# Performance work log

Measured on AMD Instinct MI355X. Metric: run time of the kernel, lower is better.

Reference implementation:

```python
import jax, jax.numpy as jnp
import numpy as np

N = 100000          # nodes
E = 3200000         # edges (avg degree 32)
EPS = 1e-5          # BatchNorm eps
SLOPE = 0.01        # LeakyReLU negative slope


def _glorot(key, shape):
    lim = float(np.sqrt(6.0 / (shape[0] + shape[1])))
    return jax.random.uniform(key, shape, jnp.float32, -lim, lim)


def setup_inputs() -> dict:
    key = jax.random.key(0)
    ks = jax.random.split(key, 8)
    x = jax.random.normal(ks[0], (N, 128), jnp.float32)
    edge_index = jax.random.randint(ks[1], (2, E), 0, N, dtype=jnp.int64)
    W1 = _glorot(ks[2], (128, 256)); b1 = jnp.zeros((256,), jnp.float32)
    W2 = _glorot(ks[3], (256, 512)); b2 = jnp.zeros((512,), jnp.float32)
    g1 = jnp.ones((256,), jnp.float32); be1 = jnp.zeros((256,), jnp.float32)
    g2 = jnp.ones((512,), jnp.float32); be2 = jnp.zeros((512,), jnp.float32)
    Wd1 = _glorot(ks[4], (512, 4096)); bd1 = jnp.zeros((4096,), jnp.float32)
    Wd2 = _glorot(ks[5], (4096, 6)); bd2 = jnp.zeros((6,), jnp.float32)
    return dict(x=x, edge_index=edge_index, W1=W1, b1=b1, W2=W2, b2=b2,
                g1=g1, be1=be1, g2=g2, be2=be2,
                Wd1=Wd1, bd1=bd1, Wd2=Wd2, bd2=bd2)


def gcn_conv(x, src, dst, W, b):
    # PyG GCNConv: x' = D^{-1/2} (A + I) D^{-1/2} (x W) + b
    n = x.shape[0]
    xw = x @ W                                   # [N, out]
    loop = jnp.arange(n, dtype=src.dtype)
    s = jnp.concatenate([src, loop])             # add self-loops
    d = jnp.concatenate([dst, loop])
    deg = jax.ops.segment_sum(jnp.ones_like(d, dtype=x.dtype), d, num_segments=n)
    dinv = jnp.where(deg > 0, jax.lax.rsqrt(deg), 0.0)
    norm = dinv[s] * dinv[d]                     # [E+N]
    out = jax.ops.segment_sum(xw[s] * norm[:, None], d, num_segments=n)
    return out + b


def batchnorm(x, g, b):
    # training-mode BN over node dim, biased variance (as torch)
    m = x.mean(axis=0)
    v = x.var(axis=0)
    return (x - m) * jax.lax.rsqrt(v + EPS) * g + b


def leaky_relu(x):
    return jnp.where(x >= 0, x, SLOPE * x)


def reference(x, edge_index, W1, b1, W2, b2, g1, be1, g2, be2, Wd1, bd1, Wd2, bd2):
    src, dst = edge_index[0], edge_index[1]
    y = leaky_relu(batchnorm(gcn_conv(x, src, dst, W1, b1), g1, be1))
    y = leaky_relu(batchnorm(gcn_conv(y, src, dst, W2, b2), g2, be2))
    y = leaky_relu(y @ Wd1 + bd1)
    y = y @ Wd2 + bd2
    return jax.nn.softmax(y, axis=1)
```

## Files before the change

### kernel.cpp

```cpp
#include <hip/hip_runtime.h>
#include <math.h>

#define LEAKY(t) ((t) >= 0.0f ? (t) : 0.01f * (t))

typedef __attribute__((ext_vector_type(8))) short bf16x8;
typedef __attribute__((ext_vector_type(4))) float f32x4;

static __device__ __forceinline__ float b2f(unsigned short u) {
    return __uint_as_float(((unsigned)u) << 16);
}
static __device__ __forceinline__ unsigned short f2b(float f) {
    unsigned x = __float_as_uint(f);
    unsigned r = (x + 0x7fffu + ((x >> 16) & 1u)) >> 16;
    return (unsigned short)r;
}


__global__ void k_seti(int* __restrict__ p, int v, int n) {
    int i = blockIdx.x * blockDim.x + threadIdx.x;
    int st = gridDim.x * blockDim.x;
    for (; i < n; i += st) p[i] = v;
}

__global__ void k_setf(float* __restrict__ p, float v, int n) {
    int i = blockIdx.x * blockDim.x + threadIdx.x;
    int st = gridDim.x * blockDim.x;
    for (; i < n; i += st) p[i] = v;
}

__global__ void k_stash_b16(const unsigned short* __restrict__ a, int i0, int i1, int i2, int i3,
                            float* __restrict__ dst) {
    if (threadIdx.x == 0 && blockIdx.x == 0) {
        dst[0] = b2f(a[i0]); dst[1] = b2f(a[i1]); dst[2] = b2f(a[i2]); dst[3] = b2f(a[i3]);
    }
}


__global__ void k_cvt(const float* __restrict__ src, unsigned short* __restrict__ dst,
                      long long n4) {
    long long i = (long long)blockIdx.x * blockDim.x + threadIdx.x;
    long long st = (long long)gridDim.x * blockDim.x;
    for (; i < n4; i += st) {
        float4 v = *(const float4*)(src + 4 * i);
        ushort4 o;
        o.x = f2b(v.x); o.y = f2b(v.y); o.z = f2b(v.z); o.w = f2b(v.w);
        *(ushort4*)(dst + 4 * i) = o;
    }
}


__global__ void k_detect(const int* __restrict__ ei, int* __restrict__ flag) {
    __shared__ int nz;
    if (threadIdx.x == 0) nz = 0;
    __syncthreads();
    int acc = 0;
    for (int i = threadIdx.x; i < 1024; i += 256) acc |= ei[2 * i + 1];
    if (acc != 0) atomicOr(&nz, 1);
    __syncthreads();
    if (threadIdx.x == 0) *flag = (nz == 0) ? 1 : 0;
}


__global__ void k_count(const int* __restrict__ ei, int E, int Nn,
                        const int* __restrict__ flag, int* __restrict__ cnt) {
    int f = *flag;
    int i = blockIdx.x * blockDim.x + threadIdx.x;
    int stride = gridDim.x * blockDim.x;
    for (; i < E; i += stride) {
        int d = f ? ei[2 * E + 2 * i] : ei[E + i];
        if ((unsigned)d < (unsigned)Nn) atomicAdd(&cnt[d], 1);
    }
}

__global__ void k_dinv(const int* __restrict__ cnt, float* __restrict__ dinv, int n) {
    int i = blockIdx.x * blockDim.x + threadIdx.x;
    if (i < n) dinv[i] = rsqrtf((float)(cnt[i] + 1));
}

__global__ void k_scan(const int* __restrict__ cnt, int* __restrict__ start, int n) {
    __shared__ int sm[256];
    __shared__ int carry;
    int tid = threadIdx.x;
    if (tid == 0) carry = 0;
    __syncthreads();
    for (int base = 0; base < n; base += 1024) {
        int i0 = base + tid * 4;
        int v0 = (i0 + 0 < n) ? cnt[i0 + 0] : 0;
        int v1 = (i0 + 1 < n) ? cnt[i0 + 1] : 0;
        int v2 = (i0 + 2 < n) ? cnt[i0 + 2] : 0;
        int v3 = (i0 + 3 < n) ? cnt[i0 + 3] : 0;
        int s = v0 + v1 + v2 + v3;
        sm[tid] = s;
        __syncthreads();
        int x = s;
        for (int off = 1; off < 256; off <<= 1) {
            int y = (tid >= off) ? sm[tid - off] : 0;
            __syncthreads();
            x += y;
            sm[tid] = x;
            __syncthreads();
        }
        int e = x - s + carry;
        if (i0 + 0 < n) start[i0 + 0] = e; e += v0;
        if (i0 + 1 < n) start[i0 + 1] = e; e += v1;
        if (i0 + 2 < n) start[i0 + 2] = e; e += v2;
        if (i0 + 3 < n) start[i0 + 3] = e; e += v3;
        __syncthreads();
        if (tid == 255) carry += sm[255];
        __syncthreads();
    }
    if (tid == 0) start[n] = carry;
}

__global__ void k_copy_i32(const int* __restrict__ a, int* __restrict__ b, int n) {
    int i = blockIdx.x * blockDim.x + threadIdx.x;
    if (i < n) b[i] = a[i];
}

__global__ void k_fill(const int* __restrict__ ei, int E, int Nn,
                       const int* __restrict__ flag,
                       int* __restrict__ cursor, int* __restrict__ srcS) {
    int f = *flag;
    int i = blockIdx.x * blockDim.x + threadIdx.x;
    int stride = gridDim.x * blockDim.x;
    for (; i < E; i += stride) {
        int s = f ? ei[2 * i] : ei[i];
        int d = f ? ei[2 * E + 2 * i] : ei[E + i];
        if ((unsigned)d < (unsigned)Nn) {
            int p = atomicAdd(&cursor[d], 1);
            srcS[p] = ((unsigned)s < (unsigned)Nn) ? s : 0;
        }
    }
}


__global__ void k_aggb(const unsigned short* __restrict__ X, const float* __restrict__ dinv,
                       const int* __restrict__ start, const int* __restrict__ srcS,
                       unsigned short* __restrict__ out, int F, int M) {
    int t = threadIdx.x;
    for (int n = blockIdx.x; n < M; n += gridDim.x) {
        float di = dinv[n];
        unsigned v = *(const unsigned*)(X + (size_t)n * F + 2 * t);
        float a0 = b2f((unsigned short)(v & 0xffff)) * di;
        float a1 = b2f((unsigned short)(v >> 16)) * di;
        int j = start[n], e1 = start[n + 1];
        for (; j + 1 < e1; j += 2) {
            int s0 = srcS[j], s1 = srcS[j + 1];
            float w0 = dinv[s0], w1 = dinv[s1];
            unsigned u0 = *(const unsigned*)(X + (size_t)s0 * F + 2 * t);
            unsigned u1 = *(const unsigned*)(X + (size_t)s1 * F + 2 * t);
            a0 += b2f((unsigned short)(u0 & 0xffff)) * w0;
            a1 += b2f((unsigned short)(u0 >> 16)) * w0;
            a0 += b2f((unsigned short)(u1 & 0xffff)) * w1;
            a1 += b2f((unsigned short)(u1 >> 16)) * w1;
        }
        if (j < e1) {
            int s0 = srcS[j];
            float w0 = dinv[s0];
            unsigned u0 = *(const unsigned*)(X + (size_t)s0 * F + 2 * t);
            a0 += b2f((unsigned short)(u0 & 0xffff)) * w0;
            a1 += b2f((unsigned short)(u0 >> 16)) * w0;
        }
        unsigned o = (unsigned)f2b(a0 * di) | ((unsigned)f2b(a1 * di) << 16);
        *(unsigned*)(out + (size_t)n * F + 2 * t) = o;
    }
}


__global__ __launch_bounds__(256, 2)
void k_gemm1(const unsigned short* __restrict__ A, const unsigned short* __restrict__ W1s,
             unsigned short* __restrict__ C, int M) {
    int tid = threadIdx.x;
    int lane = tid & 63, w = tid >> 6;
    int lr = lane & 15, lg = lane >> 4;
    int row0 = blockIdx.x * 64;
    int arow = row0 + w * 16 + lr;
    const unsigned short* Ar = A + (size_t)(arow < M ? arow : (M - 1)) * 128;
    bf16x8 a8[4];
#pragma unroll
    for (int ko = 0; ko < 4; ko++)
        a8[ko] = *(const bf16x8*)(Ar + ko * 32 + lg * 8);
    for (int ct = 0; ct < 16; ct += 2) {
        f32x4 acc0 = {0.f, 0.f, 0.f, 0.f}, acc1 = {0.f, 0.f, 0.f, 0.f};
#pragma unroll
        for (int ko = 0; ko < 4; ko++) {
            const unsigned short* bp = W1s + ((size_t)(ct * 4 + ko) * 64 + lane) * 8;
            bf16x8 b0 = *(const bf16x8*)bp;
            bf16x8 b1 = *(const bf16x8*)(bp + 2048);
            acc0 = __builtin_amdgcn_mfma_f32_16x16x32_bf16(a8[ko], b0, acc0, 0, 0, 0);
            acc1 = __builtin_amdgcn_mfma_f32_16x16x32_bf16(a8[ko], b1, acc1, 0, 0, 0);
        }
        int col = ct * 16 + lr;
#pragma unroll
        for (int i = 0; i < 4; i++) {
            int r = row0 + w * 16 + lg * 4 + i;
            if (r < M) {
                C[(size_t)r * 256 + col] = f2b(acc0[i]);
                C[(size_t)r * 256 + col + 16] = f2b(acc1[i]);
            }
        }
    }
}


__global__ void k_gemm2stats(const unsigned short* __restrict__ T2,
                             const unsigned short* __restrict__ W2s,
                             float* __restrict__ sums, int M) {
    __shared__ float ls[512];
    __shared__ float lq[512];
    int tid = threadIdx.x;
    int lane = tid & 63, w = tid >> 6;
    int lr = lane & 15, lg = lane >> 4;
    int row0 = blockIdx.x * 64;
    for (int i = tid; i < 512; i += 256) { ls[i] = 0.f; lq[i] = 0.f; }
    __syncthreads();

    int arow = row0 + w * 16 + lr;
    bf16x8 a8[8];
    if (arow < M) {
        const unsigned short* T2r = T2 + (size_t)arow * 256;
#pragma unroll
        for (int ko = 0; ko < 8; ko++)
            a8[ko] = *(const bf16x8*)(T2r + ko * 32 + lg * 8);
    } else {
#pragma unroll
        for (int ko = 0; ko < 8; ko++)
            a8[ko] = (bf16x8){0, 0, 0, 0, 0, 0, 0, 0};
    }

    for (int ct = 0; ct < 32; ct += 2) {
        f32x4 acc0 = {0.f, 0.f, 0.f, 0.f}, acc1 = {0.f, 0.f, 0.f, 0.f};
#pragma unroll
        for (int ko = 0; ko < 8; ko++) {
            const unsigned short* bp = W2s + ((size_t)(ct * 8 + ko) * 64 + lane) * 8;
            bf16x8 b0 = *(const bf16x8*)bp;
            bf16x8 b1 = *(const bf16x8*)(bp + 4096);
            acc0 = __builtin_amdgcn_mfma_f32_16x16x32_bf16(a8[ko], b0, acc0, 0, 0, 0);
            acc1 = __builtin_amdgcn_mfma_f32_16x16x32_bf16(a8[ko], b1, acc1, 0, 0, 0);
        }
        float s0 = 0.f, q0 = 0.f, s1 = 0.f, q1 = 0.f;
#pragma unroll
        for (int i = 0; i < 4; i++) {
            float y0 = acc0[i]; s0 += y0; q0 += y0 * y0;
            float y1 = acc1[i]; s1 += y1; q1 += y1 * y1;
        }
        s0 += __shfl_xor(s0, 16); s0 += __shfl_xor(s0, 32);
        q0 += __shfl_xor(q0, 16); q0 += __shfl_xor(q0, 32);
        s1 += __shfl_xor(s1, 16); s1 += __shfl_xor(s1, 32);
        q1 += __shfl_xor(q1, 16); q1 += __shfl_xor(q1, 32);
        if (lg == 0) {
            atomicAdd(&ls[ct * 16 + lr], s0);
            atomicAdd(&lq[ct * 16 + lr], q0);
            atomicAdd(&ls[(ct + 1) * 16 + lr], s1);
            atomicAdd(&lq[(ct + 1) * 16 + lr], q1);
        }
    }
    __syncthreads();
    for (int c = tid; c < 512; c += 256) {
        atomicAdd(&sums[c], ls[c]);
        atomicAdd(&sums[512 + c], lq[c]);
    }
}


__global__ void k_bnparam(float* __restrict__ sums, const float* __restrict__ g,
                          const float* __restrict__ be, int n, int F) {
    int c = blockIdx.x * blockDim.x + threadIdx.x;
    if (c < F) {
        float m = sums[c] / n;
        float v = sums[F + c] / n - m * m;
        float a = g[c] * rsqrtf(v + 1e-5f);
        sums[c] = a;
        sums[F + c] = be[c] - m * a;
    }
}

__global__ void k_colstats_b16(const unsigned short* __restrict__ X, float* __restrict__ sums, int n) {
    int t = threadIdx.x;
    int r0 = blockIdx.x * 256;
    int r1 = min(r0 + 256, n);
    float s = 0.f, q = 0.f;
    for (int r = r0; r < r1; r++) {
        float v = b2f(X[(size_t)r * 256 + t]);
        s += v; q += v * v;
    }
    atomicAdd(&sums[t], s);
    atomicAdd(&sums[256 + t], q);
}

__global__ void k_bnleaky_b16(unsigned short* __restrict__ X, const float* __restrict__ p,
                              long long total) {
    long long i = (long long)blockIdx.x * blockDim.x + threadIdx.x;
    long long stride = (long long)gridDim.x * blockDim.x;
    for (; i < total; i += stride) {
        int c = (int)(i & 255);
        float y = b2f(X[i]) * p[c] + p[256 + c];
        X[i] = f2b(LEAKY(y));
    }
}


__global__ void k_swz(const float* __restrict__ src, unsigned short* __restrict__ dst,
                      int N, int KO) {
    __shared__ float t[32][65];
    int tid = threadIdx.x;
    int ko = blockIdx.x;
    int n0 = blockIdx.y * 64;
    int r = tid >> 3, c8 = (tid & 7) * 8;
    const float* s = src + (size_t)(ko * 32 + r) * N + n0 + c8;
    float4 v0 = *(const float4*)s;
    float4 v1 = *(const float4*)(s + 4);
    t[r][c8 + 0] = v0.x; t[r][c8 + 1] = v0.y; t[r][c8 + 2] = v0.z; t[r][c8 + 3] = v0.w;
    t[r][c8 + 4] = v1.x; t[r][c8 + 5] = v1.y; t[r][c8 + 6] = v1.z; t[r][c8 + 7] = v1.w;
    __syncthreads();
    int cc = tid >> 6, lane = tid & 63;
    int lr = lane & 15, lg = lane >> 4;
    int ct = (n0 >> 4) + cc;
    bf16x8 ov;
#pragma unroll
    for (int j = 0; j < 8; j++) ov[j] = (short)f2b(t[lg * 8 + j][cc * 16 + lr]);
    *(bf16x8*)(dst + ((size_t)(ct * KO + ko) * 64 + lane) * 8) = ov;
}


__global__ __launch_bounds__(512, 1)
void k_dense(const unsigned short* __restrict__ T2,
             const unsigned short* __restrict__ W2s,
             const float* __restrict__ bnp,
             const float* __restrict__ bd1,
             const unsigned short* __restrict__ Wd1s,
             const float* __restrict__ Wd2,
             float* __restrict__ logits, int M) {
    __shared__ unsigned short Y2f[8 * 8192];
    __shared__ float sl[2][128][6];
    int tid = threadIdx.x;
    int lane = tid & 63, w = tid >> 6;
    int lr = lane & 15, lg = lane >> 4;
    int row0 = blockIdx.x * 128;

    int arow = row0 + w * 16 + lr;
    const unsigned short* T2r = T2 + (size_t)(arow < M ? arow : (M - 1)) * 256;
    bf16x8 a8[8];
#pragma unroll
    for (int ko = 0; ko < 8; ko++)
        a8[ko] = *(const bf16x8*)(T2r + ko * 32 + lg * 8);
    for (int ct = 0; ct < 32; ct += 2) {
        f32x4 acc0 = {0.f, 0.f, 0.f, 0.f}, acc1 = {0.f, 0.f, 0.f, 0.f};
#pragma unroll
        for (int ko = 0; ko < 8; ko++) {
            const unsigned short* bp = W2s + ((size_t)(ct * 8 + ko) * 64 + lane) * 8;
            bf16x8 b0 = *(const bf16x8*)bp;
            bf16x8 b1 = *(const bf16x8*)(bp + 4096);
            acc0 = __builtin_amdgcn_mfma_f32_16x16x32_bf16(a8[ko], b0, acc0, 0, 0, 0);
            acc1 = __builtin_amdgcn_mfma_f32_16x16x32_bf16(a8[ko], b1, acc1, 0, 0, 0);
        }
        int col = ct * 16 + lr;
        float sc0 = bnp[col], sh0 = bnp[512 + col];
        float sc1 = bnp[col + 16], sh1 = bnp[512 + col + 16];
        int koa = ct >> 1;
        int lgb = lr >> 3;
        int jj = lr & 7;
        int base = w * 8192 + (koa * 64 + lgb * 16) * 8 + jj;
#pragma unroll
        for (int i = 0; i < 4; i++) {
            int r16 = lg * 4 + i;
            float y0 = fmaf(acc0[i], sc0, sh0); y0 = LEAKY(y0);
            Y2f[base + r16 * 8] = f2b(y0);
            float y1 = fmaf(acc1[i], sc1, sh1); y1 = LEAKY(y1);
            Y2f[base + (32 * 8) + r16 * 8] = f2b(y1);
        }
    }
    __syncthreads();

    int rg = w & 3, ch = w >> 2;
    const unsigned short* fA = Y2f + (size_t)(2 * rg) * 8192;
    const unsigned short* fB = Y2f + (size_t)(2 * rg + 1) * 8192;
    float l0[4][6] = {{0.f}}, l1[4][6] = {{0.f}};
    int ct0 = ch * 128;
    for (int ct = ct0; ct < ct0 + 128; ct += 2) {
        f32x4 aA0 = {0.f, 0.f, 0.f, 0.f}, aA1 = {0.f, 0.f, 0.f, 0.f};
        f32x4 aB0 = {0.f, 0.f, 0.f, 0.f}, aB1 = {0.f, 0.f, 0.f, 0.f};
#pragma unroll
        for (int ko = 0; ko < 16; ko++) {
            const unsigned short* bp = Wd1s + ((size_t)(ct * 16 + ko) * 64 + lane) * 8;
            bf16x8 b0 = *(const bf16x8*)bp;
            bf16x8 b1 = *(const bf16x8*)(bp + 8192);
            bf16x8 pa = *(const bf16x8*)(fA + (ko * 64 + lane) * 8);
            bf16x8 pb = *(const bf16x8*)(fB + (ko * 64 + lane) * 8);
            aA0 = __builtin_amdgcn_mfma_f32_16x16x32_bf16(pa, b0, aA0, 0, 0, 0);
            aA1 = __builtin_amdgcn_mfma_f32_16x16x32_bf16(pa, b1, aA1, 0, 0, 0);
            aB0 = __builtin_amdgcn_mfma_f32_16x16x32_bf16(pb, b0, aB0, 0, 0, 0);
            aB1 = __builtin_amdgcn_mfma_f32_16x16x32_bf16(pb, b1, aB1, 0, 0, 0);
        }
#define EPI(C, AA, BB) { \
        int col = (ct + (C)) * 16 + lr; \
        float bv = bd1[col]; \
        const float* w2r = Wd2 + (size_t)col * 6; \
        float u0 = w2r[0], u1 = w2r[1], u2 = w2r[2]; \
        float u3 = w2r[3], u4 = w2r[4], u5 = w2r[5]; \
        _Pragma("unroll") \
        for (int i = 0; i < 4; i++) { \
            float t0 = AA[i] + bv; t0 = LEAKY(t0); \
            l0[i][0] = fmaf(t0, u0, l0[i][0]); \
            l0[i][1] = fmaf(t0, u1, l0[i][1]); \
            l0[i][2] = fmaf(t0, u2, l0[i][2]); \
            l0[i][3] = fmaf(t0, u3, l0[i][3]); \
            l0[i][4] = fmaf(t0, u4, l0[i][4]); \
            l0[i][5] = fmaf(t0, u5, l0[i][5]); \
            float t1 = BB[i] + bv; t1 = LEAKY(t1); \
            l1[i][0] = fmaf(t1, u0, l1[i][0]); \
            l1[i][1] = fmaf(t1, u1, l1[i][1]); \
            l1[i][2] = fmaf(t1, u2, l1[i][2]); \
            l1[i][3] = fmaf(t1, u3, l1[i][3]); \
            l1[i][4] = fmaf(t1, u4, l1[i][4]); \
            l1[i][5] = fmaf(t1, u5, l1[i][5]); \
        } }
        EPI(0, aA0, aB0)
        EPI(1, aA1, aB1)
#undef EPI
    }
#pragma unroll
    for (int i = 0; i < 4; i++) {
#pragma unroll
        for (int o = 0; o < 6; o++) {
            float v0 = l0[i][o];
            v0 += __shfl_xor(v0, 1); v0 += __shfl_xor(v0, 2);
            v0 += __shfl_xor(v0, 4); v0 += __shfl_xor(v0, 8);
            float v1 = l1[i][o];
            v1 += __shfl_xor(v1, 1); v1 += __shfl_xor(v1, 2);
            v1 += __shfl_xor(v1, 4); v1 += __shfl_xor(v1, 8);
            if (lr == 0) {
                sl[ch][rg * 32 + lg * 4 + i][o] = v0;
                sl[ch][rg * 32 + 16 + lg * 4 + i][o] = v1;
            }
        }
    }
    __syncthreads();
    for (int i = tid; i < 768; i += 512) {
        int r = i / 6, o = i - r * 6;
        if (row0 + r < M)
            logits[(size_t)(row0 + r) * 6 + o] = sl[0][r][o] + sl[1][r][o];
    }
}


__global__ void k_softmax(const float* __restrict__ logits, const float* __restrict__ bd2,
                          float* __restrict__ out, int M) {
    int n = blockIdx.x * blockDim.x + threadIdx.x;
    if (n >= M) return;
    float l[6];
    float mx = -1e30f;
#pragma unroll
    for (int o = 0; o < 6; o++) {
        l[o] = logits[(size_t)n * 6 + o] + bd2[o];
        mx = fmaxf(mx, l[o]);
    }
    float s = 0.f;
#pragma unroll
    for (int o = 0; o < 6; o++) { l[o] = expf(l[o] - mx); s += l[o]; }
    float inv = 1.f / s;
#pragma unroll
    for (int o = 0; o < 6; o++) out[(size_t)n * 6 + o] = l[o] * inv;
}


__global__ void k_diag_ws(float* __restrict__ out, unsigned long long ws) {
    if (threadIdx.x == 0 && blockIdx.x == 0) {
        float f = (float)((double)ws / 1099511627776.0);
        if (f > 0.999f) f = 0.999f;
        out[0] = ldexpf(1.0f + f, 34);
    }
}

__global__ void k_diag(const int* __restrict__ eflag, const int* __restrict__ startM,
                       int E, const float* __restrict__ stash,
                       const float* __restrict__ logits, float* __restrict__ out) {
    if (threadIdx.x != 0 || blockIdx.x != 0) return;
    int b1 = *eflag;
    int b2 = (*startM == E) ? 1 : 0;
    int b3 = (fabsf(stash[0] - stash[1]) > 1e-12f || fabsf(stash[2] - stash[3]) > 1e-12f) ? 1 : 0;
    int b4 = (fabsf(stash[4]) > 1e-12f || fabsf(stash[5]) > 1e-12f ||
              fabsf(stash[6]) > 1e-12f || fabsf(stash[7]) > 1e-12f) ? 1 : 0;
    float d0 = fabsf(logits[0] - logits[6]);
    float d1 = fabsf(logits[0] - logits[1]);
    int b5 = (d0 > 1e-12f && d1 > 1e-12f) ? 1 : 0;
    if (b2 && b3 && b4 && b5) return;
    float meanabs = 0.f;
    for (int i = 0; i < 16; i++) meanabs += fabsf(logits[i]);
    meanabs *= (1.f / 16.f);
    int m = (int)(32.f + 8.f * log2f(meanabs + 1e-30f));
    m = m < 0 ? 0 : (m > 127 ? 127 : m);
    int Ee = 96 + 16 * b1 + 8 * b2 + 4 * b3 + 2 * b4 + b5;
    out[0] = ldexpf(1.0f + (float)m / 128.0f, Ee - 30);
}


extern "C" void kernel_launch(void* const* d_in, const int* in_sizes, int n_in,
                              void* d_out, int out_size, void* d_ws, size_t ws_size,
                              hipStream_t stream) {
    const float* x   = (const float*)d_in[0];
    const int*   ei  = (const int*)d_in[1];
    const float* W1  = (const float*)d_in[2];
    const float* W2  = (const float*)d_in[4];
    const float* g1  = (const float*)d_in[6];
    const float* be1 = (const float*)d_in[7];
    const float* g2  = (const float*)d_in[8];
    const float* be2 = (const float*)d_in[9];
    const float* Wd1 = (const float*)d_in[10];
    const float* bd1 = (const float*)d_in[11];
    const float* Wd2 = (const float*)d_in[12];
    const float* bd2 = (const float*)d_in[13];
    float* out = (float*)d_out;

    const int M = in_sizes[0] / 128;
    const int E = in_sizes[1] / 2;

    size_t szA = (size_t)M * 512;
    size_t szB = (size_t)M * 512;
    size_t csr = (size_t)M * 8 + ((size_t)M + 1) * 8 + (size_t)E * 4 + 8192 + 128 + 66000;
    size_t need = szA + szB + csr;

    if (ws_size < need) {
        k_setf<<<2048, 256, 0, stream>>>(out, 0.f, out_size);
        k_diag_ws<<<1, 64, 0, stream>>>(out, (unsigned long long)ws_size);
        return;
    }

    char* base = (char*)d_ws;
    unsigned short* xb  = (unsigned short*)base;
    unsigned short* T1b = (unsigned short*)base + (size_t)M * 128;
    unsigned short* T2  = (unsigned short*)base;
    unsigned short* Y1 = (unsigned short*)(base + szA);
    float* logits = (float*)(base + szA);
    unsigned short* W2s  = (unsigned short*)(base + szA + (size_t)8 * 1024 * 1024);
    unsigned short* Wd1s = (unsigned short*)(base + szA + (size_t)12 * 1024 * 1024);
    char* cb = base + szA + szB;
    float* dinv   = (float*)cb;
    int*   cnt    = (int*)(dinv + M);
    int*   startA = cnt + M;
    int*   cursor = startA + (M + 1);
    int*   srcS   = cursor + (M + 1);
    float* sums   = (float*)(srcS + E);
    int*   eflag  = (int*)(sums + 2048);
    float* stash  = (float*)(eflag + 8);
    unsigned short* W1s = (unsigned short*)(((uintptr_t)(stash + 16) + 63) & ~(uintptr_t)63);

    int mt  = (M + 63) / 64;
    int mt2 = (M + 127) / 128;
    int nb  = (M + 255) / 256;

    k_detect<<<1, 256, 0, stream>>>(ei, eflag);
    k_seti<<<2048, 256, 0, stream>>>(cnt, 0, M);
    k_count<<<4096, 256, 0, stream>>>(ei, E, M, eflag, cnt);
    k_dinv<<<nb, 256, 0, stream>>>(cnt, dinv, M);
    k_scan<<<1, 256, 0, stream>>>(cnt, startA, M);
    k_copy_i32<<<nb, 256, 0, stream>>>(startA, cursor, M);
    k_fill<<<4096, 256, 0, stream>>>(ei, E, M, eflag, cursor, srcS);
    k_cvt<<<2048, 256, 0, stream>>>(x, xb, (long long)M * 32);
    k_swz<<<dim3(4, 4), 256, 0, stream>>>(W1, W1s, 256, 4);

    k_aggb<<<8192, 64, 0, stream>>>(xb, dinv, startA, srcS, T1b, 128, M);
    k_stash_b16<<<1, 64, 0, stream>>>(T1b, 3, 128 * 7 + 3, 1, 128 * 7, stash);
    k_gemm1<<<mt, 256, 0, stream>>>(T1b, W1s, Y1, M);
    k_setf<<<8, 256, 0, stream>>>(sums, 0.f, 2048);
    k_colstats_b16<<<nb, 256, 0, stream>>>(Y1, sums, M);
    k_bnparam<<<1, 256, 0, stream>>>(sums, g1, be1, M, 256);
    k_bnleaky_b16<<<4096, 256, 0, stream>>>(Y1, sums, (long long)M * 256);
    k_stash_b16<<<1, 64, 0, stream>>>(Y1, 5, 77, 256 + 5, 256 * 9 + 5, stash + 4);

    k_aggb<<<4096, 128, 0, stream>>>(Y1, dinv, startA, srcS, T2, 256, M);
    k_swz<<<dim3(8, 8), 256, 0, stream>>>(W2, W2s, 512, 8);
    k_swz<<<dim3(16, 64), 256, 0, stream>>>(Wd1, Wd1s, 4096, 16);
    k_setf<<<8, 256, 0, stream>>>(sums, 0.f, 2048);
    k_gemm2stats<<<mt, 256, 0, stream>>>(T2, W2s, sums, M);
    k_bnparam<<<2, 256, 0, stream>>>(sums, g2, be2, M, 512);

    k_dense<<<mt2, 512, 0, stream>>>(T2, W2s, sums, bd1, Wd1s, Wd2, logits, M);
    k_softmax<<<nb, 256, 0, stream>>>(logits, bd2, out, M);

    k_diag<<<1, 64, 0, stream>>>(eflag, startA + M, E, stash, logits, out);
}
```

Measured before the change: 2.464 ms.

## Fuse BN1 stats into GEMM1, BN+LeakyReLU into layer-2 gather, widen dense tile

Column sum and sum-of-squares for the first BatchNorm are now accumulated in the GEMM1 epilogue with shuffles and LDS atomics, which removes the separate column-stats pass over Y1. The normalize-plus-LeakyReLU pass is dropped: the layer-2 aggregation applies scale, shift and LeakyReLU to each gathered neighbor row as it reads it. This saves two full read/write sweeps of the N×256 tensor, but the per-edge arithmetic repeats for every incoming edge. Separately, the dense kernel now processes four column tiles per iteration instead of two, reusing each A fragment across more MFMAs at the cost of more registers. Statistics come from fp32 accumulators rather than rounded bf16 values, so results can differ slightly.

```diff
diff --git a/kernel.cpp b/kernel.cpp
--- a/kernel.cpp
+++ b/kernel.cpp
@@ -167,19 +167,68 @@
 }
 
 
+__global__ void k_agg2f(const unsigned short* __restrict__ Y1, const float* __restrict__ dinv,
+                        const int* __restrict__ start, const int* __restrict__ srcS,
+                        const float* __restrict__ bnp, unsigned short* __restrict__ T2, int M) {
+    int t = threadIdx.x;
+    float sc0 = bnp[2 * t], sc1 = bnp[2 * t + 1];
+    float sh0 = bnp[256 + 2 * t], sh1 = bnp[256 + 2 * t + 1];
+    for (int n = blockIdx.x; n < M; n += gridDim.x) {
+        float di = dinv[n];
+        unsigned v = *(const unsigned*)(Y1 + (size_t)n * 256 + 2 * t);
+        float y0 = fmaf(b2f((unsigned short)(v & 0xffff)), sc0, sh0); y0 = LEAKY(y0);
+        float y1 = fmaf(b2f((unsigned short)(v >> 16)), sc1, sh1); y1 = LEAKY(y1);
+        float a0 = y0 * di, a1 = y1 * di;
+        int j = start[n], e1 = start[n + 1];
+        for (; j + 1 < e1; j += 2) {
+            int s0 = srcS[j], s1 = srcS[j + 1];
+            float w0 = dinv[s0], w1 = dinv[s1];
+            unsigned u0 = *(const unsigned*)(Y1 + (size_t)s0 * 256 + 2 * t);
+            unsigned u1 = *(const unsigned*)(Y1 + (size_t)s1 * 256 + 2 * t);
+            float p0 = fmaf(b2f((unsigned short)(u0 & 0xffff)), sc0, sh0); p0 = LEAKY(p0);
+            float p1 = fmaf(b2f((unsigned short)(u0 >> 16)), sc1, sh1); p1 = LEAKY(p1);
+            a0 = fmaf(p0, w0, a0); a1 = fmaf(p1, w0, a1);
+            float q0 = fmaf(b2f((unsigned short)(u1 & 0xffff)), sc0, sh0); q0 = LEAKY(q0);
+            float q1 = fmaf(b2f((unsigned short)(u1 >> 16)), sc1, sh1); q1 = LEAKY(q1);
+            a0 = fmaf(q0, w1, a0); a1 = fmaf(q1, w1, a1);
+        }
+        if (j < e1) {
+            int s0 = srcS[j];
+            float w0 = dinv[s0];
+            unsigned u0 = *(const unsigned*)(Y1 + (size_t)s0 * 256 + 2 * t);
+            float p0 = fmaf(b2f((unsigned short)(u0 & 0xffff)), sc0, sh0); p0 = LEAKY(p0);
+            float p1 = fmaf(b2f((unsigned short)(u0 >> 16)), sc1, sh1); p1 = LEAKY(p1);
+            a0 = fmaf(p0, w0, a0); a1 = fmaf(p1, w0, a1);
+        }
+        unsigned o = (unsigned)f2b(a0 * di) | ((unsigned)f2b(a1 * di) << 16);
+        *(unsigned*)(T2 + (size_t)n * 256 + 2 * t) = o;
+    }
+}
+
+
 __global__ __launch_bounds__(256, 2)
 void k_gemm1(const unsigned short* __restrict__ A, const unsigned short* __restrict__ W1s,
-             unsigned short* __restrict__ C, int M) {
+             unsigned short* __restrict__ C, float* __restrict__ sums, int M) {
+    __shared__ float ls[256];
+    __shared__ float lq[256];
     int tid = threadIdx.x;
     int lane = tid & 63, w = tid >> 6;
     int lr = lane & 15, lg = lane >> 4;
     int row0 = blockIdx.x * 64;
+    ls[tid] = 0.f; lq[tid] = 0.f;
+    __syncthreads();
     int arow = row0 + w * 16 + lr;
-    const unsigned short* Ar = A + (size_t)(arow < M ? arow : (M - 1)) * 128;
     bf16x8 a8[4];
-#pragma unroll
-    for (int ko = 0; ko < 4; ko++)
-        a8[ko] = *(const bf16x8*)(Ar + ko * 32 + lg * 8);
+    if (arow < M) {
+        const unsigned short* Ar = A + (size_t)arow * 128;
+#pragma unroll
+        for (int ko = 0; ko < 4; ko++)
+            a8[ko] = *(const bf16x8*)(Ar + ko * 32 + lg * 8);
+    } else {
+#pragma unroll
+        for (int ko = 0; ko < 4; ko++)
+            a8[ko] = (bf16x8){0, 0, 0, 0, 0, 0, 0, 0};
+    }
     for (int ct = 0; ct < 16; ct += 2) {
         f32x4 acc0 = {0.f, 0.f, 0.f, 0.f}, acc1 = {0.f, 0.f, 0.f, 0.f};
 #pragma unroll
@@ -191,6 +240,7 @@
             acc1 = __builtin_amdgcn_mfma_f32_16x16x32_bf16(a8[ko], b1, acc1, 0, 0, 0);
         }
         int col = ct * 16 + lr;
+        float s0 = 0.f, q0 = 0.f, s1 = 0.f, q1 = 0.f;
 #pragma unroll
         for (int i = 0; i < 4; i++) {
             int r = row0 + w * 16 + lg * 4 + i;
@@ -198,8 +248,23 @@
                 C[(size_t)r * 256 + col] = f2b(acc0[i]);
                 C[(size_t)r * 256 + col + 16] = f2b(acc1[i]);
             }
-        }
-    }
+            float y0 = acc0[i]; s0 += y0; q0 += y0 * y0;
+            float y1 = acc1[i]; s1 += y1; q1 += y1 * y1;
+        }
+        s0 += __shfl_xor(s0, 16); s0 += __shfl_xor(s0, 32);
+        q0 += __shfl_xor(q0, 16); q0 += __shfl_xor(q0, 32);
+        s1 += __shfl_xor(s1, 16); s1 += __shfl_xor(s1, 32);
+        q1 += __shfl_xor(q1, 16); q1 += __shfl_xor(q1, 32);
+        if (lg == 0) {
+            atomicAdd(&ls[col], s0);
+            atomicAdd(&lq[col], q0);
+            atomicAdd(&ls[col + 16], s1);
+            atomicAdd(&lq[col + 16], q1);
+        }
+    }
+    __syncthreads();
+    atomicAdd(&sums[tid], ls[tid]);
+    atomicAdd(&sums[256 + tid], lq[tid]);
 }
 
 
@@ -272,30 +337,6 @@
         float a = g[c] * rsqrtf(v + 1e-5f);
         sums[c] = a;
         sums[F + c] = be[c] - m * a;
-    }
-}
-
-__global__ void k_colstats_b16(const unsigned short* __restrict__ X, float* __restrict__ sums, int n) {
-    int t = threadIdx.x;
-    int r0 = blockIdx.x * 256;
-    int r1 = min(r0 + 256, n);
-    float s = 0.f, q = 0.f;
-    for (int r = r0; r < r1; r++) {
-        float v = b2f(X[(size_t)r * 256 + t]);
-        s += v; q += v * v;
-    }
-    atomicAdd(&sums[t], s);
-    atomicAdd(&sums[256 + t], q);
-}
-
-__global__ void k_bnleaky_b16(unsigned short* __restrict__ X, const float* __restrict__ p,
-                              long long total) {
-    long long i = (long long)blockIdx.x * blockDim.x + threadIdx.x;
-    long long stride = (long long)gridDim.x * blockDim.x;
-    for (; i < total; i += stride) {
-        int c = (int)(i & 255);
-        float y = b2f(X[i]) * p[c] + p[256 + c];
-        X[i] = f2b(LEAKY(y));
     }
 }
 
@@ -377,20 +418,28 @@
     const unsigned short* fB = Y2f + (size_t)(2 * rg + 1) * 8192;
     float l0[4][6] = {{0.f}}, l1[4][6] = {{0.f}};
     int ct0 = ch * 128;
-    for (int ct = ct0; ct < ct0 + 128; ct += 2) {
+    for (int ct = ct0; ct < ct0 + 128; ct += 4) {
         f32x4 aA0 = {0.f, 0.f, 0.f, 0.f}, aA1 = {0.f, 0.f, 0.f, 0.f};
+        f32x4 aA2 = {0.f, 0.f, 0.f, 0.f}, aA3 = {0.f, 0.f, 0.f, 0.f};
         f32x4 aB0 = {0.f, 0.f, 0.f, 0.f}, aB1 = {0.f, 0.f, 0.f, 0.f};
+        f32x4 aB2 = {0.f, 0.f, 0.f, 0.f}, aB3 = {0.f, 0.f, 0.f, 0.f};
 #pragma unroll
         for (int ko = 0; ko < 16; ko++) {
             const unsigned short* bp = Wd1s + ((size_t)(ct * 16 + ko) * 64 + lane) * 8;
             bf16x8 b0 = *(const bf16x8*)bp;
             bf16x8 b1 = *(const bf16x8*)(bp + 8192);
+            bf16x8 b2 = *(const bf16x8*)(bp + 16384);
+            bf16x8 b3 = *(const bf16x8*)(bp + 24576);
             bf16x8 pa = *(const bf16x8*)(fA + (ko * 64 + lane) * 8);
             bf16x8 pb = *(const bf16x8*)(fB + (ko * 64 + lane) * 8);
             aA0 = __builtin_amdgcn_mfma_f32_16x16x32_bf16(pa, b0, aA0, 0, 0, 0);
             aA1 = __builtin_amdgcn_mfma_f32_16x16x32_bf16(pa, b1, aA1, 0, 0, 0);
+            aA2 = __builtin_amdgcn_mfma_f32_16x16x32_bf16(pa, b2, aA2, 0, 0, 0);
+            aA3 = __builtin_amdgcn_mfma_f32_16x16x32_bf16(pa, b3, aA3, 0, 0, 0);
             aB0 = __builtin_amdgcn_mfma_f32_16x16x32_bf16(pb, b0, aB0, 0, 0, 0);
             aB1 = __builtin_amdgcn_mfma_f32_16x16x32_bf16(pb, b1, aB1, 0, 0, 0);
+            aB2 = __builtin_amdgcn_mfma_f32_16x16x32_bf16(pb, b2, aB2, 0, 0, 0);
+            aB3 = __builtin_amdgcn_mfma_f32_16x16x32_bf16(pb, b3, aB3, 0, 0, 0);
         }
 #define EPI(C, AA, BB) { \
         int col = (ct + (C)) * 16 + lr; \
@@ -417,6 +466,8 @@
         } }
         EPI(0, aA0, aB0)
         EPI(1, aA1, aB1)
+        EPI(2, aA2, aB2)
+        EPI(3, aA3, aB3)
 #undef EPI
     }
 #pragma unroll
@@ -561,14 +612,12 @@
 
     k_aggb<<<8192, 64, 0, stream>>>(xb, dinv, startA, srcS, T1b, 128, M);
     k_stash_b16<<<1, 64, 0, stream>>>(T1b, 3, 128 * 7 + 3, 1, 128 * 7, stash);
-    k_gemm1<<<mt, 256, 0, stream>>>(T1b, W1s, Y1, M);
     k_setf<<<8, 256, 0, stream>>>(sums, 0.f, 2048);
-    k_colstats_b16<<<nb, 256, 0, stream>>>(Y1, sums, M);
+    k_gemm1<<<mt, 256, 0, stream>>>(T1b, W1s, Y1, sums, M);
     k_bnparam<<<1, 256, 0, stream>>>(sums, g1, be1, M, 256);
-    k_bnleaky_b16<<<4096, 256, 0, stream>>>(Y1, sums, (long long)M * 256);
     k_stash_b16<<<1, 64, 0, stream>>>(Y1, 5, 77, 256 + 5, 256 * 9 + 5, stash + 4);
 
-    k_aggb<<<4096, 128, 0, stream>>>(Y1, dinv, startA, srcS, T2, 256, M);
+    k_agg2f<<<4096, 128, 0, stream>>>(Y1, dinv, startA, srcS, sums, T2, M);
     k_swz<<<dim3(8, 8), 256, 0, stream>>>(W2, W2s, 512, 8);
     k_swz<<<dim3(16, 64), 256, 0, stream>>>(Wd1, Wd1s, 4096, 16);
     k_setf<<<8, 256, 0, stream>>>(sums, 0.f, 2048);
```

Result: slower. 3.132 ms (+27.1%).
